# Optimization experiments

Measured on AMD Instinct MI355X. Metric: run time of the kernel, lower is better.

## Reference

```python
import jax, jax.numpy as jnp
import numpy as np

N_NODES = 50000
N_EDGES = 800000
F_IN = 128
HID = 128  # hidden_dim * num_heads with num_heads=1
N_GRAPHS = 32
N_LAYERS = 4
NEG_SLOPE = 0.2
LN_EPS = 1e-5


def setup_inputs() -> dict:
    key = jax.random.key(0)
    ks = jax.random.split(key, 20)
    x = jax.random.normal(ks[0], (N_NODES, F_IN), dtype=jnp.float32)
    edge_index = jax.random.randint(ks[1], (2, N_EDGES), 0, N_NODES, dtype=jnp.int32)
    batch = jnp.sort(jax.random.randint(ks[2], (N_NODES,), 0, N_GRAPHS, dtype=jnp.int32))
    s = 0.05
    Ws = jax.random.normal(ks[3], (N_LAYERS, F_IN, HID), dtype=jnp.float32) * s
    a_src = jax.random.normal(ks[4], (N_LAYERS, HID), dtype=jnp.float32) * s
    a_dst = jax.random.normal(ks[5], (N_LAYERS, HID), dtype=jnp.float32) * s
    gat_b = jnp.zeros((N_LAYERS, HID), dtype=jnp.float32)
    ln_g = jnp.ones((N_LAYERS, HID), dtype=jnp.float32)
    ln_b = jnp.zeros((N_LAYERS, HID), dtype=jnp.float32)
    skip_W = jax.random.normal(ks[6], (F_IN, HID), dtype=jnp.float32) * s
    skip_b = jnp.zeros((HID,), dtype=jnp.float32)
    W1 = jax.random.normal(ks[7], (2 * HID, HID), dtype=jnp.float32) * s
    b1 = jnp.zeros((HID,), dtype=jnp.float32)
    W2 = jax.random.normal(ks[8], (HID, HID // 2), dtype=jnp.float32) * s
    b2 = jnp.zeros((HID // 2,), dtype=jnp.float32)
    W3 = jax.random.normal(ks[9], (HID // 2, 4), dtype=jnp.float32) * s
    b3 = jnp.zeros((4,), dtype=jnp.float32)
    return dict(x=x, edge_index=edge_index, batch=batch, Ws=Ws, a_src=a_src,
                a_dst=a_dst, gat_b=gat_b, ln_g=ln_g, ln_b=ln_b,
                skip_W=skip_W, skip_b=skip_b, W1=W1, b1=b1, W2=W2, b2=b2, W3=W3, b3=b3)


def _gat_layer(x, W, a_s, a_d, b, src, dst, n_nodes):
    # linear transform (single head)
    h = x @ W                                  # [N, C]
    e_src = h @ a_s                            # [N]
    e_dst = h @ a_d                            # [N]
    e = jax.nn.leaky_relu(e_src[src] + e_dst[dst], NEG_SLOPE)  # [E']
    # segment softmax over destination nodes
    m = jax.ops.segment_max(e, dst, num_segments=n_nodes)      # [N]
    p = jnp.exp(e - m[dst])
    z = jax.ops.segment_sum(p, dst, num_segments=n_nodes)      # [N]
    alpha = p / z[dst]                                         # [E']
    out = jax.ops.segment_sum(h[src] * alpha[:, None], dst, num_segments=n_nodes)
    return out + b


def _layernorm(x, g, b):
    mu = jnp.mean(x, axis=-1, keepdims=True)
    var = jnp.var(x, axis=-1, keepdims=True)
    return (x - mu) * jax.lax.rsqrt(var + LN_EPS) * g + b


def reference(x, edge_index, batch, Ws, a_src, a_dst, gat_b, ln_g, ln_b,
              skip_W, skip_b, W1, b1, W2, b2, W3, b3):
    n = x.shape[0]
    # PyG GATConv default: add self loops
    loops = jnp.arange(n, dtype=edge_index.dtype)
    src = jnp.concatenate([edge_index[0], loops])
    dst = jnp.concatenate([edge_index[1], loops])

    skip = x @ skip_W + skip_b
    h = x
    for i in range(N_LAYERS):
        h_new = _gat_layer(h, Ws[i], a_src[i], a_dst[i], gat_b[i], src, dst, n)
        h_new = _layernorm(h_new, ln_g[i], ln_b[i])
        if i < N_LAYERS - 1:
            h_new = jax.nn.elu(h_new)
        h = h_new + (skip if i == 0 else h)
    # global mean + max pool over graphs
    bidx = batch
    cnt = jax.ops.segment_sum(jnp.ones((n,), h.dtype), bidx, num_segments=N_GRAPHS)
    x_mean = jax.ops.segment_sum(h, bidx, num_segments=N_GRAPHS) / jnp.maximum(cnt, 1.0)[:, None]
    x_max = jax.ops.segment_max(h, bidx, num_segments=N_GRAPHS)
    g = jnp.concatenate([x_mean, x_max], axis=1)           # [G, 2*HID]
    g = jax.nn.relu(g @ W1 + b1)
    g = jax.nn.relu(g @ W2 + b2)
    return g @ W3 + b3
```

## Files before the change

### kernel.cpp

```cpp
#include <hip/hip_runtime.h>
#include <hip/hip_fp16.h>
#include <math.h>

#define NND 50000
#define NE  800000
#define HID 128
#define NGR 32
#define NLAYER 4
#define NBK 196
#define NBLK 831
#define NITEM (NE + NND)

typedef _Float16 half8 __attribute__((ext_vector_type(8)));
typedef float float4v __attribute__((ext_vector_type(4)));

static __device__ __forceinline__ unsigned fenc(float f){
  unsigned u = __float_as_uint(f);
  return (u & 0x80000000u) ? ~u : (u | 0x80000000u);
}
static __device__ __forceinline__ float fdec(unsigned u){
  return __uint_as_float((u & 0x80000000u) ? (u & 0x7fffffffu) : ~u);
}


__global__ __launch_bounds__(256) void k_count(const float* __restrict__ Ws, const float* __restrict__ skip_W,
    _Float16* __restrict__ wth, const int* __restrict__ ei, unsigned short* __restrict__ cnts)
{
  if (blockIdx.x < 5) {
    int m = blockIdx.x;
    const float* src = (m < 4) ? (Ws + (size_t)m * 16384) : skip_W;
    _Float16* oh = wth + (size_t)m * 16384;
    for (int i = threadIdx.x; i < 16384; i += 256){
      int c = i >> 7, k = i & 127;
      oh[i] = (_Float16)src[k * 128 + c];
    }
    return;
  }
  int blk = blockIdx.x - 5;
  __shared__ unsigned h[NBK];
  for (int i = threadIdx.x; i < NBK; i += 256) h[i] = 0;
  __syncthreads();
  int e0 = blk * 1024 + threadIdx.x;
#pragma unroll
  for (int i = 0; i < 4; ++i) {
    int e = e0 + i * 256;
    if (e < NITEM) {
      int d = (e < NE) ? ei[NE + e] : (e - NE);
      atomicAdd(&h[d >> 8], 1u);
    }
  }
  __syncthreads();
  for (int i = threadIdx.x; i < NBK; i += 256)
    cnts[(size_t)i * NBLK + blk] = (unsigned short)h[i];
}

__global__ __launch_bounds__(256) void k_scan1(const unsigned short* __restrict__ cnts,
    unsigned* __restrict__ offs, unsigned* __restrict__ totals)
{
  int b = blockIdx.x;
  int t = threadIdx.x;
  int lane = t & 63, wid = t >> 6;
  unsigned v[4];
  int i0 = t * 4;
#pragma unroll
  for (int k = 0; k < 4; ++k) {
    int i = i0 + k;
    v[k] = (i < NBLK) ? (unsigned)cnts[(size_t)b * NBLK + i] : 0u;
  }
  unsigned cs = v[0] + v[1] + v[2] + v[3];
  unsigned incl = cs;
#pragma unroll
  for (int o = 1; o < 64; o <<= 1) { unsigned u = __shfl_up(incl, o); if (lane >= o) incl += u; }
  __shared__ unsigned wsum[4];
  if (lane == 63) wsum[wid] = incl;
  __syncthreads();
  unsigned wbase = 0;
#pragma unroll
  for (int k = 0; k < 4; ++k) if (k < wid) wbase += wsum[k];
  unsigned run = wbase + incl - cs;
#pragma unroll
  for (int k = 0; k < 4; ++k) {
    int i = i0 + k;
    if (i < NBLK) offs[(size_t)b * NBLK + i] = run;
    run += v[k];
  }
  if (t == 255) totals[b] = wbase + incl;
}

__global__ __launch_bounds__(256) void k_scan2(const unsigned* __restrict__ totals, unsigned* __restrict__ base)
{
  int t = threadIdx.x;
  int lane = t & 63, wid = t >> 6;
  unsigned v = (t < NBK) ? totals[t] : 0u;
  unsigned incl = v;
#pragma unroll
  for (int o = 1; o < 64; o <<= 1) { unsigned u = __shfl_up(incl, o); if (lane >= o) incl += u; }
  __shared__ unsigned wsum[4];
  if (lane == 63) wsum[wid] = incl;
  __syncthreads();
  unsigned wbase = 0;
#pragma unroll
  for (int k = 0; k < 4; ++k) if (k < wid) wbase += wsum[k];
  if (t < NBK) base[t] = wbase + incl - v;
  if (t == 255) base[NBK] = wbase + incl;
}

__global__ __launch_bounds__(256) void k_scatter(const int* __restrict__ ei, const unsigned* __restrict__ offs,
    const unsigned* __restrict__ base, unsigned* __restrict__ ebuf)
{
  int blk = blockIdx.x;
  __shared__ unsigned cur[NBK];
  for (int i = threadIdx.x; i < NBK; i += 256)
    cur[i] = base[i] + offs[(size_t)i * NBLK + blk];
  __syncthreads();
  int e0 = blk * 1024 + threadIdx.x;
#pragma unroll
  for (int i = 0; i < 4; ++i) {
    int e = e0 + i * 256;
    if (e < NITEM) {
      int s, d;
      if (e < NE) { s = ei[e]; d = ei[NE + e]; } else { s = e - NE; d = e - NE; }
      unsigned pos = atomicAdd(&cur[d >> 8], 1u);
      ebuf[pos] = ((unsigned)d << 16) | (unsigned)s;
    }
  }
}

__global__ __launch_bounds__(256) void k_fine(const unsigned* __restrict__ ebuf, const unsigned* __restrict__ base,
    unsigned* __restrict__ starts, unsigned short* __restrict__ srcs, int N)
{
  int b = blockIdx.x;
  int t = threadIdx.x;
  unsigned lo = base[b], hi = base[b + 1];
  int d0 = b << 8;
  __shared__ unsigned h[256], st[256], wsum[4];
  h[t] = 0;
  __syncthreads();
  for (unsigned i = lo + t; i < hi; i += 256)
    atomicAdd(&h[(ebuf[i] >> 16) - d0], 1u);
  __syncthreads();
  unsigned v = h[t];
  int lane = t & 63, wid = t >> 6;
  unsigned incl = v;
#pragma unroll
  for (int o = 1; o < 64; o <<= 1) { unsigned u = __shfl_up(incl, o); if (lane >= o) incl += u; }
  if (lane == 63) wsum[wid] = incl;
  __syncthreads();
  unsigned wbase = 0;
#pragma unroll
  for (int k = 0; k < 4; ++k) if (k < wid) wbase += wsum[k];
  unsigned excl = wbase + incl - v;
  st[t] = excl;
  int dst = d0 + t;
  if (dst < N) starts[dst] = lo + excl;
  if (b == NBK - 1 && t == 0) starts[N] = hi;
  h[t] = 0;
  __syncthreads();
  for (unsigned i = lo + t; i < hi; i += 256) {
    unsigned w = ebuf[i];
    unsigned dl = (w >> 16) - d0;
    unsigned r = atomicAdd(&h[dl], 1u);
    srcs[lo + st[dl] + r] = (unsigned short)(w & 0xFFFFu);
  }
}

static __device__ __forceinline__ void gemm_body(int row0, const float* __restrict__ A,
    const _Float16* __restrict__ wt, const float* __restrict__ bias,
    const float* __restrict__ a_s, const float* __restrict__ a_d,
    float* __restrict__ outF, _Float16* __restrict__ outH,
    float* __restrict__ es, float* __restrict__ ed, int N)
{
  int tid = threadIdx.x;
  int w  = tid >> 6;
  int l  = tid & 63;
  int ln = l & 15;
  int q  = l >> 4;

  int row = row0 + w * 16 + ln;
  bool rok = row < N;
  const float4* Arow = (const float4*)(A + (size_t)(rok ? row : 0) * 128);

  half8 af[4];
#pragma unroll
  for (int k32 = 0; k32 < 4; ++k32) {
    int f4 = k32 * 8 + q * 2;
    float4 a0 = make_float4(0.f,0.f,0.f,0.f), a1 = a0;
    if (rok) { a0 = Arow[f4]; a1 = Arow[f4 + 1]; }
    half8 h = {(_Float16)a0.x, (_Float16)a0.y, (_Float16)a0.z, (_Float16)a0.w,
               (_Float16)a1.x, (_Float16)a1.y, (_Float16)a1.z, (_Float16)a1.w};
    af[k32] = h;
  }

  float4v acc[8];
#pragma unroll
  for (int t = 0; t < 8; ++t) acc[t] = (float4v){0.f, 0.f, 0.f, 0.f};

#pragma unroll
  for (int k32 = 0; k32 < 4; ++k32) {
    int kk = k32 * 32 + q * 8;
#pragma unroll
    for (int t = 0; t < 8; ++t) {
      half8 bv = *(const half8*)(&wt[(size_t)(t * 16 + ln) * 128 + kk]);
      acc[t] = __builtin_amdgcn_mfma_f32_16x16x32_f16(af[k32], bv, acc[t], 0, 0, 0);
    }
  }

  float bb[8];
  if (bias) {
#pragma unroll
    for (int t = 0; t < 8; ++t) bb[t] = bias[t * 16 + ln];
  }
#pragma unroll
  for (int t = 0; t < 8; ++t) {
#pragma unroll
    for (int r = 0; r < 4; ++r) {
      int gr = row0 + w * 16 + q * 4 + r;
      if (gr < N) {
        int col = t * 16 + ln;
        float v = acc[t][r] + (bias ? bb[t] : 0.f);
        if (outF) outF[(size_t)gr * 128 + col] = v;
        if (outH) outH[(size_t)gr * 128 + col] = (_Float16)v;
      }
    }
  }
  if (a_s) {
    float asv[8], adv[8];
#pragma unroll
    for (int t = 0; t < 8; ++t) { asv[t] = a_s[t * 16 + ln]; adv[t] = a_d[t * 16 + ln]; }
    float ps[4], pd[4];
#pragma unroll
    for (int r = 0; r < 4; ++r) {
      float s_ = 0.f, d_ = 0.f;
#pragma unroll
      for (int t = 0; t < 8; ++t) { s_ += acc[t][r] * asv[t]; d_ += acc[t][r] * adv[t]; }
      ps[r] = s_; pd[r] = d_;
    }
#pragma unroll
    for (int o = 1; o < 16; o <<= 1) {
#pragma unroll
      for (int r = 0; r < 4; ++r) { ps[r] += __shfl_xor(ps[r], o); pd[r] += __shfl_xor(pd[r], o); }
    }
    if (ln == 0) {
#pragma unroll
      for (int r = 0; r < 4; ++r) {
        int gr = row0 + w * 16 + q * 4 + r;
        if (gr < N) { es[gr] = ps[r]; ed[gr] = pd[r]; }
      }
    }
  }
}

__global__ __launch_bounds__(256) void gemm_mfma(const float* __restrict__ A,
    const _Float16* __restrict__ wt, const float* __restrict__ bias,
    const float* __restrict__ a_s, const float* __restrict__ a_d,
    float* __restrict__ outF, _Float16* __restrict__ outH,
    float* __restrict__ es, float* __restrict__ ed, int N)
{
  gemm_body(blockIdx.x * 64, A, wt, bias, a_s, a_d, outF, outH, es, ed, N);
}

__global__ __launch_bounds__(256) void edge_agg(
    const __half* __restrict__ hW, const float* __restrict__ es, const float* __restrict__ ed,
    const unsigned* __restrict__ starts, const unsigned short* __restrict__ srcs,
    const float* __restrict__ gb, const float* __restrict__ lg, const float* __restrict__ lb,
    const float* __restrict__ resid, float* __restrict__ hout, int do_elu, int N)
{
  __shared__ uint2 s_as[4][64];
  int wid = threadIdx.x >> 6;
  int lane = threadIdx.x & 63;
  int sub = lane >> 4;
  int sl  = lane & 15;
  int dst = blockIdx.x * 4 + wid;
  if (dst >= N) return;

  unsigned st0 = starts[dst];
  int deg = (int)(starts[dst + 1] - st0);
  float edv = ed[dst];

  float acc[8];
#pragma unroll
  for (int k = 0; k < 8; ++k) acc[k] = 0.f;
  const uint4* h4 = (const uint4*)hW;

  if (deg <= 64) {
    int s = 0;
    if (lane < deg) s = srcs[st0 + lane];
    const int PF = 4;
    uint4 qd_pre[PF];
#pragma unroll
    for (int i = 0; i < PF; ++i) {
      int idx = (i << 2) | sub;
      int sv = __shfl(s, idx);
      qd_pre[i] = make_uint4(0u, 0u, 0u, 0u);
      if (idx < deg) qd_pre[i] = h4[(size_t)sv * 16 + sl];
    }
    float x = -1e30f;
    if (lane < deg) {
      float xx = es[s] + edv;
      x = xx > 0.f ? xx : 0.2f * xx;
    }
    float m = x;
#pragma unroll
    for (int o = 32; o; o >>= 1) m = fmaxf(m, __shfl_xor(m, o));
    float p_ = (lane < deg) ? __expf(x - m) : 0.f;
    float z = p_;
#pragma unroll
    for (int o = 32; o; o >>= 1) z += __shfl_xor(z, o);
    float a_l = p_ / z;

    int iters = (deg + 3) >> 2;
#pragma unroll
    for (int i = 0; i < PF; ++i) {
      int idx = (i << 2) | sub;
      float a = __shfl(a_l, idx);
      uint4 qd = qd_pre[i];
      float2 f0 = __half22float2(*(__half2*)&qd.x);
      float2 f1 = __half22float2(*(__half2*)&qd.y);
      float2 f2 = __half22float2(*(__half2*)&qd.z);
      float2 f3 = __half22float2(*(__half2*)&qd.w);
      acc[0] += a * f0.x; acc[1] += a * f0.y;
      acc[2] += a * f1.x; acc[3] += a * f1.y;
      acc[4] += a * f2.x; acc[5] += a * f2.y;
      acc[6] += a * f3.x; acc[7] += a * f3.y;
    }
    for (int i = PF; i < iters; ++i) {
      int idx = (i << 2) | sub;
      float a = __shfl(a_l, idx);
      int sv = __shfl(s, idx);
      if (idx < deg) {
        uint4 qd = h4[(size_t)sv * 16 + sl];
        float2 f0 = __half22float2(*(__half2*)&qd.x);
        float2 f1 = __half22float2(*(__half2*)&qd.y);
        float2 f2 = __half22float2(*(__half2*)&qd.z);
        float2 f3 = __half22float2(*(__half2*)&qd.w);
        acc[0] += a * f0.x; acc[1] += a * f0.y;
        acc[2] += a * f1.x; acc[3] += a * f1.y;
        acc[4] += a * f2.x; acc[5] += a * f2.y;
        acc[6] += a * f3.x; acc[7] += a * f3.y;
      }
    }
  } else {
    float m = -1e30f;
    for (int j = lane; j < deg; j += 64) {
      float x = es[srcs[st0 + j]] + edv;
      x = x > 0.f ? x : 0.2f * x;
      m = fmaxf(m, x);
    }
#pragma unroll
    for (int o = 32; o; o >>= 1) m = fmaxf(m, __shfl_xor(m, o));
    float z = 0.f;
    for (int j = lane; j < deg; j += 64) {
      float x = es[srcs[st0 + j]] + edv;
      x = x > 0.f ? x : 0.2f * x;
      z += __expf(x - m);
    }
#pragma unroll
    for (int o = 32; o; o >>= 1) z += __shfl_xor(z, o);
    float inv_z = 1.0f / z;
    for (int c0 = 0; c0 < deg; c0 += 64) {
      int j = c0 + lane;
      int cnt = min(64, deg - c0);
      int s = 0; float p_ = 0.f;
      if (j < deg) {
        s = srcs[st0 + j];
        float x = es[s] + edv;
        x = x > 0.f ? x : 0.2f * x;
        p_ = __expf(x - m) * inv_z;
      }
      s_as[wid][lane] = make_uint2(__float_as_uint(p_), (unsigned)s);
      int iters = (cnt + 3) >> 2;
      for (int i = 0; i < iters; ++i) {
        int idx = (i << 2) | sub;
        bool valid = idx < cnt;
        uint2 av = s_as[wid][valid ? idx : 0];
        float a = valid ? __uint_as_float(av.x) : 0.f;
        uint4 qd = h4[(size_t)av.y * 16 + sl];
        float2 f0 = __half22float2(*(__half2*)&qd.x);
        float2 f1 = __half22float2(*(__half2*)&qd.y);
        float2 f2 = __half22float2(*(__half2*)&qd.z);
        float2 f3 = __half22float2(*(__half2*)&qd.w);
        acc[0] += a * f0.x; acc[1] += a * f0.y;
        acc[2] += a * f1.x; acc[3] += a * f1.y;
        acc[4] += a * f2.x; acc[5] += a * f2.y;
        acc[6] += a * f3.x; acc[7] += a * f3.y;
      }
    }
  }

#pragma unroll
  for (int k = 0; k < 8; ++k) {
    acc[k] += __shfl_xor(acc[k], 16);
    acc[k] += __shfl_xor(acc[k], 32);
  }

  float4 g0 = ((const float4*)gb)[sl * 2];
  float4 g1 = ((const float4*)gb)[sl * 2 + 1];
  float v[8];
  v[0] = acc[0] + g0.x; v[1] = acc[1] + g0.y; v[2] = acc[2] + g0.z; v[3] = acc[3] + g0.w;
  v[4] = acc[4] + g1.x; v[5] = acc[5] + g1.y; v[6] = acc[6] + g1.z; v[7] = acc[7] + g1.w;
  float s1 = 0.f, s2 = 0.f;
#pragma unroll
  for (int k = 0; k < 8; ++k) { s1 += v[k]; s2 += v[k] * v[k]; }
#pragma unroll
  for (int o = 8; o; o >>= 1) { s1 += __shfl_xor(s1, o); s2 += __shfl_xor(s2, o); }
  float mu = s1 * (1.f / 128.f);
  float var = s2 * (1.f / 128.f) - mu * mu;
  float rstd = rsqrtf(var + 1e-5f);

  float va = sub == 0 ? v[0] : (sub == 1 ? v[2] : (sub == 2 ? v[4] : v[6]));
  float vb = sub == 0 ? v[1] : (sub == 1 ? v[3] : (sub == 2 ? v[5] : v[7]));
  int col = sl * 8 + sub * 2;
  float2 Lv = *(const float2*)(lg + col);
  float2 Bv = *(const float2*)(lb + col);
  float2 Rv = *(const float2*)(resid + (long)dst * 128 + col);
  float t0 = (va - mu) * rstd * Lv.x + Bv.x;
  float t1 = (vb - mu) * rstd * Lv.y + Bv.y;
  if (do_elu) {
    t0 = t0 > 0.f ? t0 : __expf(t0) - 1.f;
    t1 = t1 > 0.f ? t1 : __expf(t1) - 1.f;
  }
  *(float2*)(hout + (long)dst * 128 + col) = make_float2(t0 + Rv.x, t1 + Rv.y);
}

__global__ __launch_bounds__(128) void k_pool(const float* __restrict__ h, const int* __restrict__ batch,
    float* __restrict__ gsum, unsigned* __restrict__ gmax, int* __restrict__ gcnt, int N)
{
  int n0 = blockIdx.x * 64;
  int c = threadIdx.x;
  int cur = -1; float ls = 0.f, lm = -1e30f; int lc = 0;
  for (int i = 0; i < 64; ++i) {
    int n = n0 + i;
    if (n >= N) break;
    int g = batch[n];
    if (g != cur) {
      if (lc > 0) {
        atomicAdd(&gsum[cur * HID + c], ls);
        atomicMax(&gmax[cur * HID + c], fenc(lm));
        if (c == 0) atomicAdd(&gcnt[cur], lc);
      }
      cur = g; ls = 0.f; lm = -1e30f; lc = 0;
    }
    float v = h[(long)n * HID + c];
    ls += v; lm = fmaxf(lm, v); lc++;
  }
  if (lc > 0) {
    atomicAdd(&gsum[cur * HID + c], ls);
    atomicMax(&gmax[cur * HID + c], fenc(lm));
    if (c == 0) atomicAdd(&gcnt[cur], lc);
  }
}

__global__ __launch_bounds__(128) void k_mlp(const float* __restrict__ gsum,
    const unsigned* __restrict__ gmax, const int* __restrict__ gcnt,
    const float* __restrict__ W1, const float* __restrict__ b1,
    const float* __restrict__ W2, const float* __restrict__ b2,
    const float* __restrict__ W3, const float* __restrict__ b3,
    float* __restrict__ out)
{
  int g = blockIdx.x;
  int c = threadIdx.x;
  __shared__ float G[256];
  __shared__ float O1[128];
  __shared__ float O2[64];
  float inv = 1.0f / fmaxf((float)gcnt[g], 1.0f);
  G[c]       = gsum[g * HID + c] * inv;
  G[128 + c] = fdec(gmax[g * HID + c]);
  __syncthreads();
  {
    float acc = 0.f;
#pragma unroll 8
    for (int k = 0; k < 256; ++k) acc += G[k] * W1[k * 128 + c];
    float v = acc + b1[c];
    O1[c] = v > 0.f ? v : 0.f;
  }
  __syncthreads();
  if (c < 64) {
    float acc = 0.f;
#pragma unroll 8
    for (int k = 0; k < 128; ++k) acc += O1[k] * W2[k * 64 + c];
    float v = acc + b2[c];
    O2[c] = v > 0.f ? v : 0.f;
  }
  __syncthreads();
  if (c < 4) {
    float acc = 0.f;
#pragma unroll 8
    for (int k = 0; k < 64; ++k) acc += O2[k] * W3[k * 4 + c];
    out[g * 4 + c] = acc + b3[c];
  }
}

extern "C" void kernel_launch(void* const* d_in, const int* in_sizes, int n_in,
                              void* d_out, int out_size, void* d_ws, size_t ws_size,
                              hipStream_t stream) {
  const float* x      = (const float*)d_in[0];
  const int*   ei     = (const int*)d_in[1];
  const int*   batch  = (const int*)d_in[2];
  const float* Ws     = (const float*)d_in[3];
  const float* a_src  = (const float*)d_in[4];
  const float* a_dst  = (const float*)d_in[5];
  const float* gat_b  = (const float*)d_in[6];
  const float* ln_g   = (const float*)d_in[7];
  const float* ln_b   = (const float*)d_in[8];
  const float* skip_W = (const float*)d_in[9];
  const float* skip_b = (const float*)d_in[10];
  const float* W1     = (const float*)d_in[11];
  const float* b1     = (const float*)d_in[12];
  const float* W2     = (const float*)d_in[13];
  const float* b2     = (const float*)d_in[14];
  const float* W3     = (const float*)d_in[15];
  const float* b3     = (const float*)d_in[16];
  float* out = (float*)d_out;

  const int N = NND;

  char* p = (char*)d_ws;
  auto alloc = [&](size_t bytes) -> void* {
    void* r = (void*)p;
    p += (bytes + 255) & ~(size_t)255;
    return r;
  };
  float*  skip  = (float*)alloc(sizeof(float) * (size_t)N * HID);
  float*  hcur  = (float*)alloc(sizeof(float) * (size_t)N * HID);
  _Float16* hW  = (_Float16*)alloc(sizeof(_Float16) * (size_t)N * HID);
  float*  es    = (float*)alloc(sizeof(float) * N);
  float*  ed    = (float*)alloc(sizeof(float) * N);
  _Float16* wth = (_Float16*)alloc(sizeof(_Float16) * 5 * 16384);
  unsigned short* cnts = (unsigned short*)alloc(sizeof(unsigned short) * (size_t)NBK * NBLK);
  unsigned* offs   = (unsigned*)alloc(sizeof(unsigned) * (size_t)NBK * NBLK);
  unsigned* totals = (unsigned*)alloc(sizeof(unsigned) * NBK);
  unsigned* base   = (unsigned*)alloc(sizeof(unsigned) * (NBK + 1));
  unsigned* ebuf   = (unsigned*)alloc(sizeof(unsigned) * (size_t)NITEM);
  unsigned* starts = (unsigned*)alloc(sizeof(unsigned) * (N + 1));
  unsigned short* srcs = (unsigned short*)alloc(sizeof(unsigned short) * (size_t)NITEM);
  char*   zbeg  = p;
  float*  gsum  = (float*)alloc(sizeof(float) * NGR * HID);
  unsigned* gmax = (unsigned*)alloc(sizeof(unsigned) * NGR * HID);
  int*    gcnt  = (int*)alloc(sizeof(int) * NGR);
  size_t zlen = (size_t)(p - zbeg);

  int gblocks = (N + 63) / 64;

  k_count  <<<5 + NBLK, 256, 0, stream>>>(Ws, skip_W, wth, ei, cnts);
  k_scan1  <<<NBK, 256, 0, stream>>>(cnts, offs, totals);
  k_scan2  <<<1, 256, 0, stream>>>(totals, base);
  k_scatter<<<NBLK, 256, 0, stream>>>(ei, offs, base, ebuf);
  k_fine   <<<NBK, 256, 0, stream>>>(ebuf, base, starts, srcs, N);

  gemm_mfma<<<gblocks, 256, 0, stream>>>(x, wth + 4 * 16384, skip_b, nullptr, nullptr,
                                         skip, nullptr, nullptr, nullptr, N);

  gemm_mfma<<<gblocks, 256, 0, stream>>>(x, wth, nullptr, a_src, a_dst,
                                         nullptr, hW, es, ed, N);
  edge_agg<<<(N + 3) / 4, 256, 0, stream>>>((const __half*)hW, es, ed, starts, srcs,
                                 gat_b, ln_g, ln_b, skip, hcur, 1, N);

  for (int l = 1; l < NLAYER; ++l) {
    gemm_mfma<<<gblocks, 256, 0, stream>>>(hcur, wth + (size_t)l * 16384, nullptr,
                                           a_src + l * HID, a_dst + l * HID,
                                           nullptr, hW, es, ed, N);
    edge_agg<<<(N + 3) / 4, 256, 0, stream>>>((const __half*)hW, es, ed, starts, srcs,
                                   gat_b + l * HID, ln_g + l * HID, ln_b + l * HID,
                                   hcur, hcur, (l < NLAYER - 1) ? 1 : 0, N);
  }

  hipMemsetAsync(zbeg, 0, zlen, stream);
  k_pool<<<(N + 63) / 64, 128, 0, stream>>>(hcur, batch, gsum, gmax, gcnt, N);
  k_mlp<<<NGR, 128, 0, stream>>>(gsum, gmax, gcnt, W1, b1, W2, b2, W3, b3, out);
}
```

Baseline: 444.0 us.

## Fuse skip and layer-0 GEMMs; feed later GEMMs fp16 activations from edge_agg

The skip projection and the first GAT linear transform now run in one kernel, so x is read and converted once and one launch is dropped. edge_agg also writes an fp16 copy of the layer output. The GEMMs for layers 1-3 read that copy in place of the fp32 hcur, halving their activation read traffic and skipping the in-kernel conversion. The cost is an extra fp16 store per node per layer, an extra buffer, and higher register use in the fused kernel with two accumulator sets.

Result: no change. 445.5 us (+0.3%).

```diff
diff --git a/kernel.cpp b/kernel.cpp
--- a/kernel.cpp
+++ b/kernel.cpp
@@ -12,6 +12,7 @@
 #define NITEM (NE + NND)
 
 typedef _Float16 half8 __attribute__((ext_vector_type(8)));
+typedef _Float16 half2v __attribute__((ext_vector_type(2)));
 typedef float float4v __attribute__((ext_vector_type(4)));
 
 static __device__ __forceinline__ unsigned fenc(float f){
@@ -164,10 +165,11 @@
   }
 }
 
-static __device__ __forceinline__ void gemm_body(int row0, const float* __restrict__ A,
-    const _Float16* __restrict__ wt, const float* __restrict__ bias,
+__global__ __launch_bounds__(256) void k_gemm2(const float* __restrict__ x,
+    const _Float16* __restrict__ wt0, const _Float16* __restrict__ wts,
+    const float* __restrict__ skip_b,
     const float* __restrict__ a_s, const float* __restrict__ a_d,
-    float* __restrict__ outF, _Float16* __restrict__ outH,
+    float* __restrict__ skip, _Float16* __restrict__ hW,
     float* __restrict__ es, float* __restrict__ ed, int N)
 {
   int tid = threadIdx.x;
@@ -175,10 +177,10 @@
   int l  = tid & 63;
   int ln = l & 15;
   int q  = l >> 4;
-
+  int row0 = blockIdx.x * 64;
   int row = row0 + w * 16 + ln;
   bool rok = row < N;
-  const float4* Arow = (const float4*)(A + (size_t)(rok ? row : 0) * 128);
+  const float4* Arow = (const float4*)(x + (size_t)(rok ? row : 0) * 128);
 
   half8 af[4];
 #pragma unroll
@@ -191,25 +193,25 @@
     af[k32] = h;
   }
 
-  float4v acc[8];
-#pragma unroll
-  for (int t = 0; t < 8; ++t) acc[t] = (float4v){0.f, 0.f, 0.f, 0.f};
+  float4v acc0[8], accs[8];
+#pragma unroll
+  for (int t = 0; t < 8; ++t) { acc0[t] = (float4v){0,0,0,0}; accs[t] = (float4v){0,0,0,0}; }
 
 #pragma unroll
   for (int k32 = 0; k32 < 4; ++k32) {
     int kk = k32 * 32 + q * 8;
 #pragma unroll
     for (int t = 0; t < 8; ++t) {
-      half8 bv = *(const half8*)(&wt[(size_t)(t * 16 + ln) * 128 + kk]);
-      acc[t] = __builtin_amdgcn_mfma_f32_16x16x32_f16(af[k32], bv, acc[t], 0, 0, 0);
+      half8 b0 = *(const half8*)(&wt0[(size_t)(t * 16 + ln) * 128 + kk]);
+      acc0[t] = __builtin_amdgcn_mfma_f32_16x16x32_f16(af[k32], b0, acc0[t], 0, 0, 0);
+      half8 bs = *(const half8*)(&wts[(size_t)(t * 16 + ln) * 128 + kk]);
+      accs[t] = __builtin_amdgcn_mfma_f32_16x16x32_f16(af[k32], bs, accs[t], 0, 0, 0);
     }
   }
 
   float bb[8];
-  if (bias) {
-#pragma unroll
-    for (int t = 0; t < 8; ++t) bb[t] = bias[t * 16 + ln];
-  }
+#pragma unroll
+  for (int t = 0; t < 8; ++t) bb[t] = skip_b[t * 16 + ln];
 #pragma unroll
   for (int t = 0; t < 8; ++t) {
 #pragma unroll
@@ -217,13 +219,12 @@
       int gr = row0 + w * 16 + q * 4 + r;
       if (gr < N) {
         int col = t * 16 + ln;
-        float v = acc[t][r] + (bias ? bb[t] : 0.f);
-        if (outF) outF[(size_t)gr * 128 + col] = v;
-        if (outH) outH[(size_t)gr * 128 + col] = (_Float16)v;
+        skip[(size_t)gr * 128 + col] = accs[t][r] + bb[t];
+        hW[(size_t)gr * 128 + col] = (_Float16)acc0[t][r];
       }
     }
   }
-  if (a_s) {
+  {
     float asv[8], adv[8];
 #pragma unroll
     for (int t = 0; t < 8; ++t) { asv[t] = a_s[t * 16 + ln]; adv[t] = a_d[t * 16 + ln]; }
@@ -232,7 +233,7 @@
     for (int r = 0; r < 4; ++r) {
       float s_ = 0.f, d_ = 0.f;
 #pragma unroll
-      for (int t = 0; t < 8; ++t) { s_ += acc[t][r] * asv[t]; d_ += acc[t][r] * adv[t]; }
+      for (int t = 0; t < 8; ++t) { s_ += acc0[t][r] * asv[t]; d_ += acc0[t][r] * adv[t]; }
       ps[r] = s_; pd[r] = d_;
     }
 #pragma unroll
@@ -250,20 +251,83 @@
   }
 }
 
-__global__ __launch_bounds__(256) void gemm_mfma(const float* __restrict__ A,
-    const _Float16* __restrict__ wt, const float* __restrict__ bias,
+__global__ __launch_bounds__(256) void gemm_h(const _Float16* __restrict__ A,
+    const _Float16* __restrict__ wt,
     const float* __restrict__ a_s, const float* __restrict__ a_d,
-    float* __restrict__ outF, _Float16* __restrict__ outH,
-    float* __restrict__ es, float* __restrict__ ed, int N)
-{
-  gemm_body(blockIdx.x * 64, A, wt, bias, a_s, a_d, outF, outH, es, ed, N);
+    _Float16* __restrict__ outH, float* __restrict__ es, float* __restrict__ ed, int N)
+{
+  int tid = threadIdx.x;
+  int w  = tid >> 6;
+  int l  = tid & 63;
+  int ln = l & 15;
+  int q  = l >> 4;
+  int row0 = blockIdx.x * 64;
+  int row = row0 + w * 16 + ln;
+  bool rok = row < N;
+  const _Float16* Arow = A + (size_t)(rok ? row : 0) * 128;
+
+  half8 hz = {(_Float16)0,(_Float16)0,(_Float16)0,(_Float16)0,
+              (_Float16)0,(_Float16)0,(_Float16)0,(_Float16)0};
+  half8 af[4];
+#pragma unroll
+  for (int k32 = 0; k32 < 4; ++k32)
+    af[k32] = rok ? *(const half8*)(Arow + k32 * 32 + q * 8) : hz;
+
+  float4v acc[8];
+#pragma unroll
+  for (int t = 0; t < 8; ++t) acc[t] = (float4v){0,0,0,0};
+
+#pragma unroll
+  for (int k32 = 0; k32 < 4; ++k32) {
+    int kk = k32 * 32 + q * 8;
+#pragma unroll
+    for (int t = 0; t < 8; ++t) {
+      half8 bv = *(const half8*)(&wt[(size_t)(t * 16 + ln) * 128 + kk]);
+      acc[t] = __builtin_amdgcn_mfma_f32_16x16x32_f16(af[k32], bv, acc[t], 0, 0, 0);
+    }
+  }
+
+#pragma unroll
+  for (int t = 0; t < 8; ++t) {
+#pragma unroll
+    for (int r = 0; r < 4; ++r) {
+      int gr = row0 + w * 16 + q * 4 + r;
+      if (gr < N) outH[(size_t)gr * 128 + t * 16 + ln] = (_Float16)acc[t][r];
+    }
+  }
+  {
+    float asv[8], adv[8];
+#pragma unroll
+    for (int t = 0; t < 8; ++t) { asv[t] = a_s[t * 16 + ln]; adv[t] = a_d[t * 16 + ln]; }
+    float ps[4], pd[4];
+#pragma unroll
+    for (int r = 0; r < 4; ++r) {
+      float s_ = 0.f, d_ = 0.f;
+#pragma unroll
+      for (int t = 0; t < 8; ++t) { s_ += acc[t][r] * asv[t]; d_ += acc[t][r] * adv[t]; }
+      ps[r] = s_; pd[r] = d_;
+    }
+#pragma unroll
+    for (int o = 1; o < 16; o <<= 1) {
+#pragma unroll
+      for (int r = 0; r < 4; ++r) { ps[r] += __shfl_xor(ps[r], o); pd[r] += __shfl_xor(pd[r], o); }
+    }
+    if (ln == 0) {
+#pragma unroll
+      for (int r = 0; r < 4; ++r) {
+        int gr = row0 + w * 16 + q * 4 + r;
+        if (gr < N) { es[gr] = ps[r]; ed[gr] = pd[r]; }
+      }
+    }
+  }
 }
 
 __global__ __launch_bounds__(256) void edge_agg(
     const __half* __restrict__ hW, const float* __restrict__ es, const float* __restrict__ ed,
     const unsigned* __restrict__ starts, const unsigned short* __restrict__ srcs,
     const float* __restrict__ gb, const float* __restrict__ lg, const float* __restrict__ lb,
-    const float* __restrict__ resid, float* __restrict__ hout, int do_elu, int N)
+    const float* __restrict__ resid, float* __restrict__ hout, _Float16* __restrict__ hA,
+    int do_elu, int N)
 {
   __shared__ uint2 s_as[4][64];
   int wid = threadIdx.x >> 6;
@@ -419,7 +483,12 @@
     t0 = t0 > 0.f ? t0 : __expf(t0) - 1.f;
     t1 = t1 > 0.f ? t1 : __expf(t1) - 1.f;
   }
-  *(float2*)(hout + (long)dst * 128 + col) = make_float2(t0 + Rv.x, t1 + Rv.y);
+  float y0 = t0 + Rv.x, y1 = t1 + Rv.y;
+  *(float2*)(hout + (long)dst * 128 + col) = make_float2(y0, y1);
+  if (hA) {
+    half2v hv = {(_Float16)y0, (_Float16)y1};
+    *(half2v*)(hA + (long)dst * 128 + col) = hv;
+  }
 }
 
 __global__ __launch_bounds__(128) void k_pool(const float* __restrict__ h, const int* __restrict__ batch,
@@ -523,6 +592,7 @@
   float*  skip  = (float*)alloc(sizeof(float) * (size_t)N * HID);
   float*  hcur  = (float*)alloc(sizeof(float) * (size_t)N * HID);
   _Float16* hW  = (_Float16*)alloc(sizeof(_Float16) * (size_t)N * HID);
+  _Float16* hA  = (_Float16*)alloc(sizeof(_Float16) * (size_t)N * HID);
   float*  es    = (float*)alloc(sizeof(float) * N);
   float*  ed    = (float*)alloc(sizeof(float) * N);
   _Float16* wth = (_Float16*)alloc(sizeof(_Float16) * 5 * 16384);
@@ -547,21 +617,19 @@
   k_scatter<<<NBLK, 256, 0, stream>>>(ei, offs, base, ebuf);
   k_fine   <<<NBK, 256, 0, stream>>>(ebuf, base, starts, srcs, N);
 
-  gemm_mfma<<<gblocks, 256, 0, stream>>>(x, wth + 4 * 16384, skip_b, nullptr, nullptr,
-                                         skip, nullptr, nullptr, nullptr, N);
-
-  gemm_mfma<<<gblocks, 256, 0, stream>>>(x, wth, nullptr, a_src, a_dst,
-                                         nullptr, hW, es, ed, N);
+  k_gemm2<<<gblocks, 256, 0, stream>>>(x, wth, wth + 4 * 16384, skip_b, a_src, a_dst,
+                                       skip, hW, es, ed, N);
   edge_agg<<<(N + 3) / 4, 256, 0, stream>>>((const __half*)hW, es, ed, starts, srcs,
-                                 gat_b, ln_g, ln_b, skip, hcur, 1, N);
+                                 gat_b, ln_g, ln_b, skip, hcur, hA, 1, N);
 
   for (int l = 1; l < NLAYER; ++l) {
-    gemm_mfma<<<gblocks, 256, 0, stream>>>(hcur, wth + (size_t)l * 16384, nullptr,
-                                           a_src + l * HID, a_dst + l * HID,
-                                           nullptr, hW, es, ed, N);
+    gemm_h<<<gblocks, 256, 0, stream>>>(hA, wth + (size_t)l * 16384,
+                                        a_src + l * HID, a_dst + l * HID,
+                                        hW, es, ed, N);
     edge_agg<<<(N + 3) / 4, 256, 0, stream>>>((const __half*)hW, es, ed, starts, srcs,
                                    gat_b + l * HID, ln_g + l * HID, ln_b + l * HID,
-                                   hcur, hcur, (l < NLAYER - 1) ? 1 : 0, N);
+                                   hcur, hcur, (l < NLAYER - 1) ? hA : (_Float16*)nullptr,
+                                   (l < NLAYER - 1) ? 1 : 0, N);
   }
 
   hipMemsetAsync(zbeg, 0, zlen, stream);
```
